# Performance work log

Hardware: AMD Instinct MI355X
Metric: run time of the kernel (lower is better)

## Reference

```python
import jax, jax.numpy as jnp
import numpy as np

B, T, D = 4, 2048, 1024
H, S = 16, 64  # n_heads, stalk_dim; D == H*S
P_ADIC_BASE = 2
MAX_VAL = 16


def quantize_6bit(x):
    # symmetric int6 quantization with straight-through estimator
    scale = jnp.max(jnp.abs(x)) / 31.0 + 1e-8
    q = jnp.clip(jnp.round(x / scale), -31, 31) * scale
    return x + jax.lax.stop_gradient(q - x)


def build_p_adic_bias(seq_len, p=2, max_val=16):
    idx = jnp.arange(seq_len)
    d = jnp.abs(idx[:, None] - idx[None, :])
    nonzero = d > 0
    vp = jnp.zeros_like(d)
    work = d
    for _ in range(max_val):  # fixed iterations; v_2(|i-j|) <= log2(T) < 16
        divisible = nonzero & (work % p == 0)
        vp = vp + divisible.astype(vp.dtype)
        work = jnp.where(divisible, work // p, work)
    vals = jnp.minimum(vp, max_val).astype(jnp.float32)
    vals = jnp.where(nonzero, vals, jnp.float32(max_val))
    return vals / max_val


def setup_inputs() -> dict:
    key = jax.random.key(0)
    ks = jax.random.split(key, 8)
    std = 0.02
    return {
        "x": jax.random.normal(ks[0], (B, T, D), dtype=jnp.float32),
        "wq": jax.random.normal(ks[1], (D, D), dtype=jnp.float32) * std,
        "wk": jax.random.normal(ks[2], (D, D), dtype=jnp.float32) * std,
        "wv": jax.random.normal(ks[3], (D, D), dtype=jnp.float32) * std,
        "wo": jax.random.normal(ks[4], (D, D), dtype=jnp.float32) * std,
        "wu": jax.random.normal(ks[5], (S, S), dtype=jnp.float32) * std,
        "wsv": jax.random.normal(ks[6], (S, S), dtype=jnp.float32) * std,
        "p_scale": jnp.ones((1,), dtype=jnp.float32) * 0.1,
    }


def reference(x, wq, wk, wv, wo, wu, wsv, p_scale):
    h, s = H, S
    scale = 1.0 / jnp.sqrt(jnp.float32(s))
    # quantized linear projections (F.linear: x @ W.T)
    Q = (x @ quantize_6bit(wq).T).reshape(B, T, h, s).transpose(0, 2, 1, 3)
    K = (x @ quantize_6bit(wk).T).reshape(B, T, h, s).transpose(0, 2, 1, 3)
    V = (x @ quantize_6bit(wv).T).reshape(B, T, h, s).transpose(0, 2, 1, 3)
    # stalk (low-rank sheaf) maps on the head dim
    Qs = Q @ quantize_6bit(wu).T
    Ks = K @ quantize_6bit(wsv).T
    scores = jnp.einsum("bhqs,bhks->bhqk", Qs, Ks) * scale
    p_bias = build_p_adic_bias(T, p=P_ADIC_BASE, max_val=MAX_VAL)
    scores = scores + p_scale[0] * p_bias[None, None, :, :]
    causal = jnp.triu(jnp.ones((T, T), dtype=bool), k=1)
    scores = jnp.where(causal[None, None], -jnp.inf, scores)
    attn = jax.nn.softmax(scores, axis=-1)
    out = jnp.einsum("bhqk,bhks->bhqs", attn, V)
    out = out.transpose(0, 2, 1, 3).reshape(B, T, D)
    return out @ quantize_6bit(wo).T
```

## Files before the change

### kernel.cpp

```cpp
#include <hip/hip_runtime.h>
#include <hip/hip_bf16.h>
#include <stdint.h>


typedef __bf16 bf16_t;
typedef __attribute__((ext_vector_type(4))) __bf16 bf16x4;
typedef __attribute__((ext_vector_type(8))) __bf16 bf16x8;
typedef __attribute__((ext_vector_type(4))) float f32x4;

#define BB 4
#define TT 2048
#define DD 1024
#define HH 16
#define SS 64

__device__ __forceinline__ float quant6(float v, float s) {
    float q = rintf(v / s);
    q = fminf(fmaxf(q, -31.0f), 31.0f);
    return q * s;
}

__device__ __forceinline__ float fexp2(float x) {
#if __has_builtin(__builtin_amdgcn_exp2f)
    return __builtin_amdgcn_exp2f(x);
#else
    return exp2f(x);
#endif
}

typedef __attribute__((address_space(3))) uint32_t lds_u32;
typedef const __attribute__((address_space(1))) uint32_t glb_u32;

__global__ __launch_bounds__(256) void ptable_kernel(const float* __restrict__ psc,
                                                     float* __restrict__ tbl) {
    const int idx = blockIdx.x * 256 + threadIdx.x;
    const int l = idx & 63, c = (idx >> 6) & 3, e = idx >> 8;
    const int l15 = l & 15, quad = l >> 4;
    const float pb2 = psc[0] * 1.44269504089f * 0.0625f;
    f32x4 v;
    #pragma unroll
    for (int r = 0; r < 4; ++r) {
        const int d = e * 16 + l15 - (c * 16 + quad * 4 + r);
        float val;
        if (d < 0) val = -INFINITY;
        else if (d == 0) val = pb2 * 16.0f;
        else val = pb2 * (float)__builtin_ctz((unsigned)d);
        v[r] = val;
    }
    *(f32x4*)(tbl + (size_t)idx * 4) = v;
}

__global__ __launch_bounds__(256) void absmax6(const float* __restrict__ wq,
                                               const float* __restrict__ wk,
                                               const float* __restrict__ wv,
                                               const float* __restrict__ wo,
                                               const float* __restrict__ wu,
                                               const float* __restrict__ wsv,
                                               float* __restrict__ amax) {
    const int t = blockIdx.y;
    const float* src = (t == 0) ? wq : (t == 1) ? wk : (t == 2) ? wv
                     : (t == 3) ? wo : (t == 4) ? wu : wsv;
    const int n4 = (t < 4) ? (1048576 / 4) : (4096 / 4);
    float m = 0.0f;
    for (int i = blockIdx.x * blockDim.x + threadIdx.x; i < n4; i += gridDim.x * blockDim.x) {
        float4 v = ((const float4*)src)[i];
        m = fmaxf(m, fmaxf(fmaxf(fabsf(v.x), fabsf(v.y)), fmaxf(fabsf(v.z), fabsf(v.w))));
    }
    #pragma unroll
    for (int mask = 32; mask > 0; mask >>= 1)
        m = fmaxf(m, __shfl_xor(m, mask));
    __shared__ float red[4];
    int w = threadIdx.x >> 6;
    if ((threadIdx.x & 63) == 0) red[w] = m;
    __syncthreads();
    if (threadIdx.x == 0) {
        m = fmaxf(fmaxf(red[0], red[1]), fmaxf(red[2], red[3]));
        atomicMax((int*)(amax + t), __float_as_int(m));
    }
}

__global__ __launch_bounds__(256) void xcvt_kernel(const float* __restrict__ x,
                                                   bf16_t* __restrict__ xb) {
    int i = (blockIdx.x * 256 + threadIdx.x) * 8;
    float4 f0 = *(const float4*)(x + i);
    float4 f1 = *(const float4*)(x + i + 4);
    bf16x8 v;
    v[0] = (bf16_t)f0.x; v[1] = (bf16_t)f0.y; v[2] = (bf16_t)f0.z; v[3] = (bf16_t)f0.w;
    v[4] = (bf16_t)f1.x; v[5] = (bf16_t)f1.y; v[6] = (bf16_t)f1.z; v[7] = (bf16_t)f1.w;
    *(bf16x8*)(xb + i) = v;
}

__global__ __launch_bounds__(256) void prep_w(const float* __restrict__ wq,
                                              const float* __restrict__ wk,
                                              const float* __restrict__ wv,
                                              const float* __restrict__ wo,
                                              const float* __restrict__ wu,
                                              const float* __restrict__ wsv,
                                              const float* __restrict__ amax,
                                              bf16_t* __restrict__ W_all,
                                              bf16_t* __restrict__ Wo) {
    const int which = blockIdx.y;
    if (blockIdx.x < 512) {
        const float* src = which ? wo : wv;
        bf16_t* dst = which ? Wo : (W_all + (size_t)2048 * 1024);
        float s = amax[which ? 3 : 2] / 31.0f + 1e-8f;
        int i = (blockIdx.x * 256 + threadIdx.x) * 8;
        float4 f0 = *(const float4*)(src + i);
        float4 f1 = *(const float4*)(src + i + 4);
        bf16x8 v;
        v[0] = (bf16_t)quant6(f0.x, s); v[1] = (bf16_t)quant6(f0.y, s);
        v[2] = (bf16_t)quant6(f0.z, s); v[3] = (bf16_t)quant6(f0.w, s);
        v[4] = (bf16_t)quant6(f1.x, s); v[5] = (bf16_t)quant6(f1.y, s);
        v[6] = (bf16_t)quant6(f1.z, s); v[7] = (bf16_t)quant6(f1.w, s);
        *(bf16x8*)(dst + i) = v;
        return;
    }
    const int fx = blockIdx.x - 512;
    const float* wbig = which ? wk : wq;
    const float* wsml = which ? wsv : wu;
    const float sb = amax[which ? 1 : 0] / 31.0f + 1e-8f;
    const float ss = amax[which ? 5 : 4] / 31.0f + 1e-8f;
    const float oscale = which ? 1.0f : 0.125f * 1.44269504089f;
    bf16_t* outp = W_all + (size_t)which * 1024 * 1024;
    const int h = fx >> 4, n0 = (fx & 15) * 64;
    const int w = threadIdx.x >> 6, l = threadIdx.x & 63;
    const int l15 = l & 15, quad = l >> 4, q8 = quad * 8;
    const int m0 = w * 16;

    bf16x8 af[2];
    #pragma unroll
    for (int kc = 0; kc < 2; ++kc) {
        const float* src = wsml + (m0 + l15) * 64 + kc * 32 + q8;
        float4 f0 = *(const float4*)(src);
        float4 f1 = *(const float4*)(src + 4);
        bf16x8 a;
        a[0] = (bf16_t)quant6(f0.x, ss); a[1] = (bf16_t)quant6(f0.y, ss);
        a[2] = (bf16_t)quant6(f0.z, ss); a[3] = (bf16_t)quant6(f0.w, ss);
        a[4] = (bf16_t)quant6(f1.x, ss); a[5] = (bf16_t)quant6(f1.y, ss);
        a[6] = (bf16_t)quant6(f1.z, ss); a[7] = (bf16_t)quant6(f1.w, ss);
        af[kc] = a;
    }
    f32x4 acc[4];
    #pragma unroll
    for (int nb = 0; nb < 4; ++nb) acc[nb] = (f32x4){0.f, 0.f, 0.f, 0.f};
    #pragma unroll
    for (int kc = 0; kc < 2; ++kc) {
        #pragma unroll
        for (int nb = 0; nb < 4; ++nb) {
            bf16x8 bfr;
            #pragma unroll
            for (int j = 0; j < 8; ++j)
                bfr[j] = (bf16_t)quant6(wbig[(size_t)(h * 64 + kc * 32 + q8 + j) * 1024 + n0 + nb * 16 + l15], sb);
            acc[nb] = __builtin_amdgcn_mfma_f32_16x16x32_bf16(af[kc], bfr, acc[nb], 0, 0, 0);
        }
    }
    #pragma unroll
    for (int nb = 0; nb < 4; ++nb)
        #pragma unroll
        for (int r = 0; r < 4; ++r)
            outp[(size_t)(h * 64 + m0 + quad * 4 + r) * 1024 + n0 + nb * 16 + l15] =
                (bf16_t)(acc[nb][r] * oscale);
}

template <bool OUT_F32>
__global__ __launch_bounds__(256) void gemm128(const bf16_t* __restrict__ A,
                                               const bf16_t* __restrict__ Bt,
                                               void* __restrict__ Cv,
                                               int lda, int ldb, int ldc, int K) {
    __shared__ __align__(16) bf16_t As[128 * 64];
    __shared__ __align__(16) bf16_t Bs[128 * 64];
    const int tid = threadIdx.x;
    const int w = tid >> 6, l = tid & 63;
    const int l15 = l & 15, quad = l >> 4;
    const int m0 = blockIdx.y * 128, n0 = blockIdx.x * 128;
    const int wm = (w & 1) * 64, wn = (w >> 1) * 64;

    f32x4 acc[4][4];
    #pragma unroll
    for (int a = 0; a < 4; ++a)
        #pragma unroll
        for (int b = 0; b < 4; ++b) acc[a][b] = (f32x4){0.f, 0.f, 0.f, 0.f};

    for (int kc = 0; kc < K; kc += 64) {
        __syncthreads();
        #pragma unroll
        for (int rep = 0; rep < 4; ++rep) {
            int ci = rep * 256 + w * 64 + l;
            int row = ci >> 3, slot = ci & 7;
            int gch = slot ^ ((row ^ (row >> 3)) & 7);
            __builtin_amdgcn_global_load_lds(
                (glb_u32*)(A + (size_t)(m0 + row) * lda + kc + gch * 8),
                (lds_u32*)(As + (rep * 256 + w * 64) * 8), 16, 0, 0);
            __builtin_amdgcn_global_load_lds(
                (glb_u32*)(Bt + (size_t)(n0 + row) * ldb + kc + gch * 8),
                (lds_u32*)(Bs + (rep * 256 + w * 64) * 8), 16, 0, 0);
        }
        __syncthreads();
        #pragma unroll
        for (int kb = 0; kb < 2; ++kb) {
            bf16x8 af[4], bfr[4];
            #pragma unroll
            for (int mb = 0; mb < 4; ++mb) {
                int row = wm + mb * 16 + l15;
                int slot = ((kb << 2) + quad) ^ ((row ^ (row >> 3)) & 7);
                af[mb] = *(const bf16x8*)(As + (row << 6) + slot * 8);
            }
            #pragma unroll
            for (int nb = 0; nb < 4; ++nb) {
                int row = wn + nb * 16 + l15;
                int slot = ((kb << 2) + quad) ^ ((row ^ (row >> 3)) & 7);
                bfr[nb] = *(const bf16x8*)(Bs + (row << 6) + slot * 8);
            }
            #pragma unroll
            for (int mb = 0; mb < 4; ++mb)
                #pragma unroll
                for (int nb = 0; nb < 4; ++nb)
                    acc[mb][nb] = __builtin_amdgcn_mfma_f32_16x16x32_bf16(af[mb], bfr[nb], acc[mb][nb], 0, 0, 0);
        }
    }
    #pragma unroll
    for (int mb = 0; mb < 4; ++mb) {
        #pragma unroll
        for (int nb = 0; nb < 4; ++nb) {
            int col = n0 + wn + nb * 16 + l15;
            #pragma unroll
            for (int r = 0; r < 4; ++r) {
                int row = m0 + wm + mb * 16 + quad * 4 + r;
                if constexpr (OUT_F32)
                    ((float*)Cv)[(size_t)row * ldc + col] = acc[mb][nb][r];
                else
                    ((bf16_t*)Cv)[(size_t)row * ldc + col] = (bf16_t)acc[mb][nb][r];
            }
        }
    }
}

__global__ __launch_bounds__(256) void vtrans_kernel(const bf16_t* __restrict__ QKV,
                                                     bf16_t* __restrict__ Vt) {
    __shared__ __align__(16) bf16_t tile[64 * 72];
    const int tid = threadIdx.x;
    const int bh = blockIdx.x >> 5, tt = blockIdx.x & 31;
    const int b = bh >> 4, h = bh & 15;
    #pragma unroll
    for (int rep = 0; rep < 2; ++rep) {
        int ci = rep * 256 + tid;
        int row = ci >> 3, ch = ci & 7;
        bf16x8 v = *(const bf16x8*)(QKV + ((size_t)(b * TT + tt * 64 + row)) * 3072 + 2048 + h * 64 + ch * 8);
        #pragma unroll
        for (int j = 0; j < 8; ++j) tile[(ch * 8 + j) * 72 + row] = v[j];
    }
    __syncthreads();
    #pragma unroll
    for (int rep = 0; rep < 2; ++rep) {
        int ci = rep * 256 + tid;
        int s = ci >> 3, ch = ci & 7;
        bf16x8 v = *(const bf16x8*)(tile + s * 72 + ch * 8);
        *(bf16x8*)(Vt + ((size_t)(bh * 64 + s)) * TT + tt * 64 + ch * 8) = v;
    }
}

__device__ __forceinline__ void attn_step(bf16_t* __restrict__ Pw,
                                          const bf16x8 kb[4][2], const bf16x8 vb[4][2],
                                          const bf16x8 qa[2], const bf16x8 ones,
                                          const f32x4 binit[4],
                                          f32x4* oacc, f32x4& lacc,
                                          int l15, int quad) {
    f32x4 sacc[4];
    #pragma unroll
    for (int c = 0; c < 4; ++c) sacc[c] = binit[c];
    #pragma unroll
    for (int kc = 0; kc < 2; ++kc)
        #pragma unroll
        for (int c = 0; c < 4; ++c)
            sacc[c] = __builtin_amdgcn_mfma_f32_16x16x32_bf16(kb[c][kc], qa[kc], sacc[c], 0, 0, 0);

    #pragma unroll
    for (int c = 0; c < 4; ++c) {
        bf16x4 pk;
        #pragma unroll
        for (int r = 0; r < 4; ++r)
            pk[r] = (bf16_t)fexp2(sacc[c][r]);
        int pp = (c * 2 + (quad >> 1)) ^ (l15 & 7);
        *(bf16x4*)(Pw + l15 * 64 + pp * 8 + (quad & 1) * 4) = pk;
    }
    __builtin_amdgcn_wave_barrier();
    #pragma unroll
    for (int kc = 0; kc < 2; ++kc) {
        bf16x8 pa = *(const bf16x8*)(Pw + l15 * 64 + (((kc * 4 + quad) ^ (l15 & 7)) * 8));
        #pragma unroll
        for (int sb = 0; sb < 4; ++sb)
            oacc[sb] = __builtin_amdgcn_mfma_f32_16x16x32_bf16(pa, vb[sb][kc], oacc[sb], 0, 0, 0);
        lacc = __builtin_amdgcn_mfma_f32_16x16x32_bf16(pa, ones, lacc, 0, 0, 0);
    }
    __builtin_amdgcn_wave_barrier();
}

__global__ __launch_bounds__(256, 2) void attn_kernel(const bf16_t* __restrict__ QKV,
                                                      const bf16_t* __restrict__ Vt,
                                                      const float* __restrict__ Bias,
                                                      bf16_t* __restrict__ O) {
    __shared__ __align__(16) bf16_t Ks[2 * 64 * 64];
    __shared__ __align__(16) bf16_t Vs[2 * 64 * 64];
    __shared__ __align__(16) bf16_t Ps[4 * 16 * 64];

    const int tid = threadIdx.x;
    const int w = tid >> 6, l = tid & 63;
    const int l15 = l & 15, quad = l >> 4, q8 = quad * 8;
    const int pair = (blockIdx.x >> 3) & 15;
    const int bh = (blockIdx.x & 7) + ((blockIdx.x >> 7) << 3);
    const int b = bh >> 4, h = bh & 15;
    const int qtA = pair, qtB = 31 - pair;
    const int q0A = qtA * 64 + w * 16, q0B = qtB * 64 + w * 16;

    const size_t xbase = (size_t)b * TT * 3072;

    bf16x8 qaA[2], qaB[2];
    #pragma unroll
    for (int kc = 0; kc < 2; ++kc) {
        qaA[kc] = *(const bf16x8*)(QKV + xbase + (size_t)(q0A + l15) * 3072 + h * 64 + kc * 32 + q8);
        qaB[kc] = *(const bf16x8*)(QKV + xbase + (size_t)(q0B + l15) * 3072 + h * 64 + kc * 32 + q8);
    }

    bf16x8 ones;
    #pragma unroll
    for (int j = 0; j < 8; ++j) ones[j] = (bf16_t)1.0f;

    f32x4 oA[4], oB[4], lA, lB;
    lA = (f32x4){0.f, 0.f, 0.f, 0.f};
    lB = (f32x4){0.f, 0.f, 0.f, 0.f};
    #pragma unroll
    for (int i = 0; i < 4; ++i) {
        oA[i] = (f32x4){0.f, 0.f, 0.f, 0.f};
        oB[i] = (f32x4){0.f, 0.f, 0.f, 0.f};
    }
    bf16_t* Pw = Ps + w * 1024;

    auto STAGE = [&](int kt, int hb) {
        #pragma unroll
        for (int rep = 0; rep < 2; ++rep) {
            int ci = rep * 256 + tid;
            int row = ci >> 3, slot = ci & 7;
            int gch = slot ^ ((row ^ (row >> 3)) & 7);
            __builtin_amdgcn_global_load_lds(
                (glb_u32*)(QKV + xbase + (size_t)(kt * 64 + row) * 3072 + 1024 + h * 64 + gch * 8),
                (lds_u32*)(Ks + hb * 4096 + (rep * 256 + w * 64) * 8), 16, 0, 0);
            __builtin_amdgcn_global_load_lds(
                (glb_u32*)(Vt + (size_t)bh * 131072 + (size_t)row * 2048 + kt * 64 + gch * 8),
                (lds_u32*)(Vs + hb * 4096 + (rep * 256 + w * 64) * 8), 16, 0, 0);
        }
    };
    auto COMPUTE = [&](int kt, int hb, const f32x4 bB[4], const f32x4 bA[4], bool doA) {
        bf16x8 kb[4][2], vb[4][2];
        #pragma unroll
        for (int kc = 0; kc < 2; ++kc) {
            #pragma unroll
            for (int c = 0; c < 4; ++c) {
                int row = c * 16 + l15;
                int slot = (kc * 4 + quad) ^ ((row ^ (row >> 3)) & 7);
                kb[c][kc] = *(const bf16x8*)(Ks + hb * 4096 + row * 64 + slot * 8);
                vb[c][kc] = *(const bf16x8*)(Vs + hb * 4096 + row * 64 + slot * 8);
            }
        }
        attn_step(Pw, kb, vb, qaB, ones, bB, oB, lB, l15, quad);
        if (doA)
            attn_step(Pw, kb, vb, qaA, ones, bA, oA, lA, l15, quad);
    };

    const int nkt = qtB + 1;
    for (int kt2 = 0; kt2 < nkt; kt2 += 2) {
        const bool has2 = (kt2 + 1) < nkt;
        __syncthreads();
        STAGE(kt2, 0);
        if (has2) STAGE(kt2 + 1, 1);
        const bool doA0 = kt2 <= qtA;
        const bool doA1 = has2 && (kt2 + 1) <= qtA;
        f32x4 bB0[4], bA0[4], bB1[4], bA1[4];
        {
            const float* bp = Bias + ((((size_t)(qtB - kt2) * 4 + w) * 4) * 64 + l) * 4;
            #pragma unroll
            for (int c = 0; c < 4; ++c) bB0[c] = *(const f32x4*)(bp + c * 256);
        }
        if (doA0) {
            const float* bp = Bias + ((((size_t)(qtA - kt2) * 4 + w) * 4) * 64 + l) * 4;
            #pragma unroll
            for (int c = 0; c < 4; ++c) bA0[c] = *(const f32x4*)(bp + c * 256);
        }
        if (has2) {
            const float* bp = Bias + ((((size_t)(qtB - kt2 - 1) * 4 + w) * 4) * 64 + l) * 4;
            #pragma unroll
            for (int c = 0; c < 4; ++c) bB1[c] = *(const f32x4*)(bp + c * 256);
        }
        if (doA1) {
            const float* bp = Bias + ((((size_t)(qtA - kt2 - 1) * 4 + w) * 4) * 64 + l) * 4;
            #pragma unroll
            for (int c = 0; c < 4; ++c) bA1[c] = *(const f32x4*)(bp + c * 256);
        }
        __syncthreads();
        COMPUTE(kt2, 0, bB0, bA0, doA0);
        if (has2) COMPUTE(kt2 + 1, 1, bB1, bA1, doA1);
    }

    #pragma unroll
    for (int t = 0; t < 2; ++t) {
        const f32x4 lc = t ? lB : lA;
        f32x4* oo = t ? oB : oA;
        int q0 = t ? q0B : q0A;
        #pragma unroll
        for (int r = 0; r < 4; ++r) {
            float invr = 1.0f / lc[r];
            #pragma unroll
            for (int sb = 0; sb < 4; ++sb) {
                int q = q0 + quad * 4 + r;
                int col = h * 64 + sb * 16 + l15;
                O[(size_t)(b * TT + q) * DD + col] = (bf16_t)(oo[sb][r] * invr);
            }
        }
    }
}

extern "C" void kernel_launch(void* const* d_in, const int* in_sizes, int n_in,
                              void* d_out, int out_size, void* d_ws, size_t ws_size,
                              hipStream_t stream) {
    const float* x   = (const float*)d_in[0];
    const float* wq  = (const float*)d_in[1];
    const float* wk  = (const float*)d_in[2];
    const float* wv  = (const float*)d_in[3];
    const float* wo  = (const float*)d_in[4];
    const float* wu  = (const float*)d_in[5];
    const float* wsv = (const float*)d_in[6];
    const float* psc = (const float*)d_in[7];
    float* out = (float*)d_out;

    char* ws = (char*)d_ws;
    float*  amax  = (float*)(ws);
    bf16_t* W_all = (bf16_t*)(ws + 256);
    bf16_t* Wo    = (bf16_t*)(ws + 6291712);
    bf16_t* xb    = (bf16_t*)(ws + 8388864);
    bf16_t* Obuf  = xb;
    bf16_t* QKV   = (bf16_t*)(ws + 25166080);
    bf16_t* Vt    = (bf16_t*)(ws + 75497728);
    float*  Bias  = (float*)(ws + 92274944);

    hipLaunchKernelGGL(ptable_kernel, dim3(128), dim3(256), 0, stream, psc, Bias);
    hipLaunchKernelGGL(absmax6, dim3(64, 6), dim3(256), 0, stream, wq, wk, wv, wo, wu, wsv, amax);
    hipLaunchKernelGGL(prep_w, dim3(768, 2), dim3(256), 0, stream,
                       wq, wk, wv, wo, wu, wsv, amax, W_all, Wo);
    hipLaunchKernelGGL(xcvt_kernel, dim3(4096), dim3(256), 0, stream, x, xb);

    hipLaunchKernelGGL((gemm128<false>), dim3(24, 64), dim3(256), 0, stream,
                       xb, W_all, (void*)QKV, 1024, 1024, 3072, 1024);

    hipLaunchKernelGGL(vtrans_kernel, dim3(2048), dim3(256), 0, stream, QKV, Vt);

    hipLaunchKernelGGL(attn_kernel, dim3(1024), dim3(256), 0, stream, QKV, Vt, Bias, Obuf);

    hipLaunchKernelGGL((gemm128<true>), dim3(8, 64), dim3(256), 0, stream,
                       Obuf, Wo, (void*)out, 1024, 1024, 1024, 1024);
}
```

Baseline: 283.2 us.

## Process four query tiles per attention block to reuse staged K/V tiles

Each attention block now handles four causal-balanced query tiles (p, 15-p, 16+p, 31-p) instead of two, and the grid is halved to 512 blocks. Each staged K/V tile is read from global memory once and reused for up to four query tiles, and the K and V fragment loads from LDS are split so only one set is live at a time. Bias loads move into the per-tile compute path. The cost is more accumulator registers (four sets of O and L), a larger P scratch buffer in LDS, and fewer blocks in flight, which may reduce occupancy and load balance.

```diff
diff --git a/kernel.cpp b/kernel.cpp
--- a/kernel.cpp
+++ b/kernel.cpp
@@ -259,81 +259,43 @@
     }
 }
 
-__device__ __forceinline__ void attn_step(bf16_t* __restrict__ Pw,
-                                          const bf16x8 kb[4][2], const bf16x8 vb[4][2],
-                                          const bf16x8 qa[2], const bf16x8 ones,
-                                          const f32x4 binit[4],
-                                          f32x4* oacc, f32x4& lacc,
-                                          int l15, int quad) {
-    f32x4 sacc[4];
-    #pragma unroll
-    for (int c = 0; c < 4; ++c) sacc[c] = binit[c];
-    #pragma unroll
-    for (int kc = 0; kc < 2; ++kc)
-        #pragma unroll
-        for (int c = 0; c < 4; ++c)
-            sacc[c] = __builtin_amdgcn_mfma_f32_16x16x32_bf16(kb[c][kc], qa[kc], sacc[c], 0, 0, 0);
-
-    #pragma unroll
-    for (int c = 0; c < 4; ++c) {
-        bf16x4 pk;
-        #pragma unroll
-        for (int r = 0; r < 4; ++r)
-            pk[r] = (bf16_t)fexp2(sacc[c][r]);
-        int pp = (c * 2 + (quad >> 1)) ^ (l15 & 7);
-        *(bf16x4*)(Pw + l15 * 64 + pp * 8 + (quad & 1) * 4) = pk;
-    }
-    __builtin_amdgcn_wave_barrier();
-    #pragma unroll
-    for (int kc = 0; kc < 2; ++kc) {
-        bf16x8 pa = *(const bf16x8*)(Pw + l15 * 64 + (((kc * 4 + quad) ^ (l15 & 7)) * 8));
-        #pragma unroll
-        for (int sb = 0; sb < 4; ++sb)
-            oacc[sb] = __builtin_amdgcn_mfma_f32_16x16x32_bf16(pa, vb[sb][kc], oacc[sb], 0, 0, 0);
-        lacc = __builtin_amdgcn_mfma_f32_16x16x32_bf16(pa, ones, lacc, 0, 0, 0);
-    }
-    __builtin_amdgcn_wave_barrier();
-}
-
 __global__ __launch_bounds__(256, 2) void attn_kernel(const bf16_t* __restrict__ QKV,
                                                       const bf16_t* __restrict__ Vt,
                                                       const float* __restrict__ Bias,
                                                       bf16_t* __restrict__ O) {
     __shared__ __align__(16) bf16_t Ks[2 * 64 * 64];
     __shared__ __align__(16) bf16_t Vs[2 * 64 * 64];
-    __shared__ __align__(16) bf16_t Ps[4 * 16 * 64];
+    __shared__ __align__(16) bf16_t Ps[4 * 4 * 16 * 64];
 
     const int tid = threadIdx.x;
     const int w = tid >> 6, l = tid & 63;
     const int l15 = l & 15, quad = l >> 4, q8 = quad * 8;
-    const int pair = (blockIdx.x >> 3) & 15;
-    const int bh = (blockIdx.x & 7) + ((blockIdx.x >> 7) << 3);
+    const int p = (blockIdx.x >> 3) & 7;
+    const int bh = (blockIdx.x & 7) + ((blockIdx.x >> 6) << 3);
     const int b = bh >> 4, h = bh & 15;
-    const int qtA = pair, qtB = 31 - pair;
-    const int q0A = qtA * 64 + w * 16, q0B = qtB * 64 + w * 16;
+    const int qt[4] = {p, 15 - p, 16 + p, 31 - p};
 
     const size_t xbase = (size_t)b * TT * 3072;
 
-    bf16x8 qaA[2], qaB[2];
-    #pragma unroll
-    for (int kc = 0; kc < 2; ++kc) {
-        qaA[kc] = *(const bf16x8*)(QKV + xbase + (size_t)(q0A + l15) * 3072 + h * 64 + kc * 32 + q8);
-        qaB[kc] = *(const bf16x8*)(QKV + xbase + (size_t)(q0B + l15) * 3072 + h * 64 + kc * 32 + q8);
-    }
+    bf16x8 qa[4][2];
+    #pragma unroll
+    for (int t = 0; t < 4; ++t)
+        #pragma unroll
+        for (int kc = 0; kc < 2; ++kc)
+            qa[t][kc] = *(const bf16x8*)(QKV + xbase + (size_t)(qt[t] * 64 + w * 16 + l15) * 3072 + h * 64 + kc * 32 + q8);
 
     bf16x8 ones;
     #pragma unroll
     for (int j = 0; j < 8; ++j) ones[j] = (bf16_t)1.0f;
 
-    f32x4 oA[4], oB[4], lA, lB;
-    lA = (f32x4){0.f, 0.f, 0.f, 0.f};
-    lB = (f32x4){0.f, 0.f, 0.f, 0.f};
-    #pragma unroll
-    for (int i = 0; i < 4; ++i) {
-        oA[i] = (f32x4){0.f, 0.f, 0.f, 0.f};
-        oB[i] = (f32x4){0.f, 0.f, 0.f, 0.f};
-    }
-    bf16_t* Pw = Ps + w * 1024;
+    f32x4 oacc[4][4], lacc[4];
+    #pragma unroll
+    for (int t = 0; t < 4; ++t) {
+        lacc[t] = (f32x4){0.f, 0.f, 0.f, 0.f};
+        #pragma unroll
+        for (int i = 0; i < 4; ++i) oacc[t][i] = (f32x4){0.f, 0.f, 0.f, 0.f};
+    }
+    bf16_t* Pw = Ps + w * 4096;
 
     auto STAGE = [&](int kt, int hb) {
         #pragma unroll
@@ -349,70 +311,89 @@
                 (lds_u32*)(Vs + hb * 4096 + (rep * 256 + w * 64) * 8), 16, 0, 0);
         }
     };
-    auto COMPUTE = [&](int kt, int hb, const f32x4 bB[4], const f32x4 bA[4], bool doA) {
-        bf16x8 kb[4][2], vb[4][2];
-        #pragma unroll
-        for (int kc = 0; kc < 2; ++kc) {
-            #pragma unroll
-            for (int c = 0; c < 4; ++c) {
-                int row = c * 16 + l15;
-                int slot = (kc * 4 + quad) ^ ((row ^ (row >> 3)) & 7);
-                kb[c][kc] = *(const bf16x8*)(Ks + hb * 4096 + row * 64 + slot * 8);
-                vb[c][kc] = *(const bf16x8*)(Vs + hb * 4096 + row * 64 + slot * 8);
-            }
-        }
-        attn_step(Pw, kb, vb, qaB, ones, bB, oB, lB, l15, quad);
-        if (doA)
-            attn_step(Pw, kb, vb, qaA, ones, bA, oA, lA, l15, quad);
+
+    auto COMPUTE = [&](int kt, int hb) {
+        {
+            bf16x8 kb[4][2];
+            #pragma unroll
+            for (int kc = 0; kc < 2; ++kc)
+                #pragma unroll
+                for (int c = 0; c < 4; ++c) {
+                    int row = c * 16 + l15;
+                    int slot = (kc * 4 + quad) ^ ((row ^ (row >> 3)) & 7);
+                    kb[c][kc] = *(const bf16x8*)(Ks + hb * 4096 + row * 64 + slot * 8);
+                }
+            #pragma unroll
+            for (int t = 0; t < 4; ++t) {
+                if (kt > qt[t]) continue;
+                const float* bp = Bias + ((((size_t)(qt[t] - kt) * 4 + w) * 4) * 64 + l) * 4;
+                f32x4 sacc[4];
+                #pragma unroll
+                for (int c = 0; c < 4; ++c) sacc[c] = *(const f32x4*)(bp + c * 256);
+                #pragma unroll
+                for (int kc = 0; kc < 2; ++kc)
+                    #pragma unroll
+                    for (int c = 0; c < 4; ++c)
+                        sacc[c] = __builtin_amdgcn_mfma_f32_16x16x32_bf16(kb[c][kc], qa[t][kc], sacc[c], 0, 0, 0);
+                #pragma unroll
+                for (int c = 0; c < 4; ++c) {
+                    bf16x4 pk;
+                    #pragma unroll
+                    for (int r = 0; r < 4; ++r)
+                        pk[r] = (bf16_t)fexp2(sacc[c][r]);
+                    int pp = (c * 2 + (quad >> 1)) ^ (l15 & 7);
+                    *(bf16x4*)(Pw + t * 1024 + l15 * 64 + pp * 8 + (quad & 1) * 4) = pk;
+                }
+            }
+        }
+        __builtin_amdgcn_wave_barrier();
+        {
+            bf16x8 vb[4][2];
+            #pragma unroll
+            for (int kc = 0; kc < 2; ++kc)
+                #pragma unroll
+                for (int c = 0; c < 4; ++c) {
+                    int row = c * 16 + l15;
+                    int slot = (kc * 4 + quad) ^ ((row ^ (row >> 3)) & 7);
+                    vb[c][kc] = *(const bf16x8*)(Vs + hb * 4096 + row * 64 + slot * 8);
+                }
+            #pragma unroll
+            for (int t = 0; t < 4; ++t) {
+                if (kt > qt[t]) continue;
+                #pragma unroll
+                for (int kc = 0; kc < 2; ++kc) {
+                    bf16x8 pa = *(const bf16x8*)(Pw + t * 1024 + l15 * 64 + (((kc * 4 + quad) ^ (l15 & 7)) * 8));
+                    #pragma unroll
+                    for (int sb = 0; sb < 4; ++sb)
+                        oacc[t][sb] = __builtin_amdgcn_mfma_f32_16x16x32_bf16(pa, vb[sb][kc], oacc[t][sb], 0, 0, 0);
+                    lacc[t] = __builtin_amdgcn_mfma_f32_16x16x32_bf16(pa, ones, lacc[t], 0, 0, 0);
+                }
+            }
+        }
+        __builtin_amdgcn_wave_barrier();
     };
 
-    const int nkt = qtB + 1;
+    const int nkt = qt[3] + 1;
     for (int kt2 = 0; kt2 < nkt; kt2 += 2) {
         const bool has2 = (kt2 + 1) < nkt;
         __syncthreads();
         STAGE(kt2, 0);
         if (has2) STAGE(kt2 + 1, 1);
-        const bool doA0 = kt2 <= qtA;
-        const bool doA1 = has2 && (kt2 + 1) <= qtA;
-        f32x4 bB0[4], bA0[4], bB1[4], bA1[4];
-        {
-            const float* bp = Bias + ((((size_t)(qtB - kt2) * 4 + w) * 4) * 64 + l) * 4;
-            #pragma unroll
-            for (int c = 0; c < 4; ++c) bB0[c] = *(const f32x4*)(bp + c * 256);
-        }
-        if (doA0) {
-            const float* bp = Bias + ((((size_t)(qtA - kt2) * 4 + w) * 4) * 64 + l) * 4;
-            #pragma unroll
-            for (int c = 0; c < 4; ++c) bA0[c] = *(const f32x4*)(bp + c * 256);
-        }
-        if (has2) {
-            const float* bp = Bias + ((((size_t)(qtB - kt2 - 1) * 4 + w) * 4) * 64 + l) * 4;
-            #pragma unroll
-            for (int c = 0; c < 4; ++c) bB1[c] = *(const f32x4*)(bp + c * 256);
-        }
-        if (doA1) {
-            const float* bp = Bias + ((((size_t)(qtA - kt2 - 1) * 4 + w) * 4) * 64 + l) * 4;
-            #pragma unroll
-            for (int c = 0; c < 4; ++c) bA1[c] = *(const f32x4*)(bp + c * 256);
-        }
         __syncthreads();
-        COMPUTE(kt2, 0, bB0, bA0, doA0);
-        if (has2) COMPUTE(kt2 + 1, 1, bB1, bA1, doA1);
-    }
-
-    #pragma unroll
-    for (int t = 0; t < 2; ++t) {
-        const f32x4 lc = t ? lB : lA;
-        f32x4* oo = t ? oB : oA;
-        int q0 = t ? q0B : q0A;
+        COMPUTE(kt2, 0);
+        if (has2) COMPUTE(kt2 + 1, 1);
+    }
+
+    #pragma unroll
+    for (int t = 0; t < 4; ++t) {
         #pragma unroll
         for (int r = 0; r < 4; ++r) {
-            float invr = 1.0f / lc[r];
+            float invr = 1.0f / lacc[t][r];
             #pragma unroll
             for (int sb = 0; sb < 4; ++sb) {
-                int q = q0 + quad * 4 + r;
+                int q = qt[t] * 64 + w * 16 + quad * 4 + r;
                 int col = h * 64 + sb * 16 + l15;
-                O[(size_t)(b * TT + q) * DD + col] = (bf16_t)(oo[sb][r] * invr);
+                O[(size_t)(b * TT + q) * DD + col] = (bf16_t)(oacc[t][sb][r] * invr);
             }
         }
     }
@@ -452,7 +433,7 @@
 
     hipLaunchKernelGGL(vtrans_kernel, dim3(2048), dim3(256), 0, stream, QKV, Vt);
 
-    hipLaunchKernelGGL(attn_kernel, dim3(1024), dim3(256), 0, stream, QKV, Vt, Bias, Obuf);
+    hipLaunchKernelGGL(attn_kernel, dim3(512), dim3(256), 0, stream, QKV, Vt, Bias, Obuf);
 
     hipLaunchKernelGGL((gemm128<true>), dim3(8, 64), dim3(256), 0, stream,
                        Obuf, Wo, (void*)out, 1024, 1024, 1024, 1024);
```

Measured after the change: 269.3 us. -4.9%, faster.
